# Optimization experiments

Hardware: AMD Instinct MI355X
Metric: run time of the kernel (lower is better)

The kernel has to match this reference:

```python
import jax, jax.numpy as jnp
import numpy as np

D = 128
BITS = 3
N_LEVELS = 1 << BITS  # 8
BATCH = 262144
EPS = 1e-8


def _rotation_matrix(skew_params):
    """Cayley map: A skew-symmetric from strict-upper-tri params, R = (I+A)^{-1}(I-A)."""
    iu = np.triu_indices(D, k=1)
    A = jnp.zeros((D, D), dtype=skew_params.dtype).at[iu].set(skew_params)
    A = A - A.T
    I = jnp.eye(D, dtype=skew_params.dtype)
    # torch.linalg.solve(I + A, I - A) -> R with (I + A) @ R = (I - A)
    return jnp.linalg.solve(I + A, I - A)


def setup_inputs() -> dict:
    key = jax.random.key(0)
    k1, k2, k3 = jax.random.split(key, 3)
    x = jax.random.normal(k1, (BATCH, D), dtype=jnp.float32)
    # small init so Cayley rotation stays well-conditioned (torch init is zeros)
    skew_params = jax.random.normal(k2, (D * (D - 1) // 2,), dtype=jnp.float32) * 0.05
    # Lloyd-Max centroids are a sorted 1-D codebook of 2^bits levels
    centroids = jnp.sort(jax.random.normal(k3, (N_LEVELS,), dtype=jnp.float32))
    running_mean = jnp.zeros((D,), dtype=jnp.float32)
    return {"x": x, "skew_params": skew_params, "centroids": centroids,
            "running_mean": running_mean}


def reference(x, skew_params, centroids, running_mean):
    R = _rotation_matrix(skew_params)                      # (D, D) orthogonal
    mean = jax.lax.stop_gradient(running_mean)             # buffer, detached in torch
    x_c = x - mean                                         # (B, D)
    norms = jnp.maximum(jnp.linalg.norm(x_c, axis=-1, keepdims=True), EPS)
    x_unit = x_c / norms
    x_rot = x_unit @ R.T                                   # rotate
    # STE quantize: argmin-distance gather == one_hot @ centroids
    idx = jnp.argmin(jnp.abs(x_rot[..., None] - centroids), axis=-1)  # (B, D)
    x_quant = x_rot - jax.lax.stop_gradient(x_rot) + jnp.take(centroids, idx)
    x_recon = (x_quant @ R) * norms + mean                 # unrotate, rescale, recenter
    return x_recon
```

## Files before the change

### kernel.cpp

```cpp
#include <hip/hip_runtime.h>

#define BATCH 262144
#define MARGIN 1e-5f
#define LIST_CAP (1u<<20)

typedef __attribute__((ext_vector_type(8))) short short8;
typedef __attribute__((ext_vector_type(16))) float f32x16;


__device__ __forceinline__ unsigned f2bf(float f) {
  unsigned u = __float_as_uint(f);
  return (u + 0x7FFFu + ((u >> 16) & 1u)) >> 16;
}

__global__ __attribute__((amdgpu_waves_per_eu(4, 4))) __launch_bounds__(1024)
void kpre(const float* __restrict__ skew, const float* __restrict__ x,
          const float* __restrict__ mean, double* __restrict__ M64,
          double* __restrict__ Y64, float* __restrict__ normg,
          float* __restrict__ invg, unsigned int* __restrict__ counter)
{
  const int tid = threadIdx.x;

  if (blockIdx.x != 0) {
    const int b  = blockIdx.x - 1;
    const int wv = tid >> 6, ln = tid & 63;
    const int rowbase = b*1024 + wv*64;
    const float2 mv = *(const float2*)(mean + 2*ln);
    for (int i = 0; i < 64; ++i) {
      const int row = rowbase + i;
      float2 xv = *(const float2*)(x + (size_t)row*128 + 2*ln);
      float a = xv.x - mv.x, c = xv.y - mv.y;
      float sq = fmaf(a, a, c*c);
      sq += __shfl_xor(sq, 1);  sq += __shfl_xor(sq, 2);  sq += __shfl_xor(sq, 4);
      sq += __shfl_xor(sq, 8);  sq += __shfl_xor(sq, 16); sq += __shfl_xor(sq, 32);
      if (ln == 0) {
        float n = fmaxf(sqrtf(sq), 1e-8f);
        normg[row] = n;
        invg[row]  = 1.0f / n;
      }
    }
    return;
  }

  __shared__ float colk[2][128];
  __shared__ float pivrow[128];
  const int i = tid >> 3;
  const int s = tid & 7;
  if (tid == 0) *counter = 0;

  float M[16];
  #pragma unroll
  for (int e = 0; e < 16; ++e) {
    int j = s + 8*e;
    float v;
    if (i == j)      v = 1.0f;
    else if (i < j)  v =  skew[i*127 - (i*(i-1))/2 + (j - i - 1)];
    else             v = -skew[j*127 - (j*(j-1))/2 + (i - j - 1)];
    M[e] = v;
    M64[i*128 + j] = (double)v;
  }
  if (s == 0) colk[0][i] = M[0];
  __syncthreads();

  for (int k = 0; k < 128; ++k) {
    const int p = k & 1, np = p ^ 1;
    const int ns = (k + 1) & 7, ne = (k + 1) >> 3;
    if (i == k) {
      float rec = 1.0f / colk[p][k];
      #pragma unroll
      for (int e = 0; e < 16; ++e) {
        int j = s + 8*e;
        float v = (j == k) ? 1.0f : M[e];
        v *= rec;
        M[e] = v;
        pivrow[j] = v;
      }
      if (s == ns && k < 127) colk[np][i] = M[ne];
    }
    __syncthreads();
    if (i != k) {
      float f = colk[p][i];
      #pragma unroll
      for (int e = 0; e < 16; ++e) {
        int j = s + 8*e;
        float v = (j == k) ? 0.0f : M[e];
        M[e] = fmaf(-f, pivrow[j], v);
      }
      if (s == ns && k < 127) colk[np][i] = M[ne];
    }
    __syncthreads();
  }

  #pragma unroll
  for (int e = 0; e < 16; ++e) {
    int j = s + 8*e;
    Y64[i*128 + j] = (double)M[e];
  }
}

__global__ __launch_bounds__(256, 2)
void kref(const double* __restrict__ M64, const double* __restrict__ Yin,
          double* __restrict__ Yout, double* __restrict__ Rt64,
          unsigned short* __restrict__ img, const int final_pass)
{
  __shared__ double Yc[128][17];
  __shared__ double T[128][17];
  const int t = threadIdx.x;
  const int c0 = blockIdx.x * 16;

  #pragma unroll
  for (int u = 0; u < 8; ++u) {
    int idx = u*256 + t;
    int row = idx >> 4, cc = idx & 15;
    Yc[row][cc] = Yin[row*128 + c0 + cc];
  }
  __syncthreads();

  const int m = t >> 1;
  const int h = (t & 1) * 8;

  double a0=0,a1=0,a2=0,a3=0,a4=0,a5=0,a6=0,a7=0;
  for (int j = 0; j < 128; ++j) {
    double mv = M64[m*128 + j];
    a0 = fma(mv, Yc[j][h+0], a0);  a1 = fma(mv, Yc[j][h+1], a1);
    a2 = fma(mv, Yc[j][h+2], a2);  a3 = fma(mv, Yc[j][h+3], a3);
    a4 = fma(mv, Yc[j][h+4], a4);  a5 = fma(mv, Yc[j][h+5], a5);
    a6 = fma(mv, Yc[j][h+6], a6);  a7 = fma(mv, Yc[j][h+7], a7);
  }
  T[m][h+0]=a0; T[m][h+1]=a1; T[m][h+2]=a2; T[m][h+3]=a3;
  T[m][h+4]=a4; T[m][h+5]=a5; T[m][h+6]=a6; T[m][h+7]=a7;
  __syncthreads();

  double b0=0,b1=0,b2=0,b3=0,b4=0,b5=0,b6=0,b7=0;
  for (int j = 0; j < 128; ++j) {
    double yv = Yin[m*128 + j];
    b0 = fma(yv, T[j][h+0], b0);  b1 = fma(yv, T[j][h+1], b1);
    b2 = fma(yv, T[j][h+2], b2);  b3 = fma(yv, T[j][h+3], b3);
    b4 = fma(yv, T[j][h+4], b4);  b5 = fma(yv, T[j][h+5], b5);
    b6 = fma(yv, T[j][h+6], b6);  b7 = fma(yv, T[j][h+7], b7);
  }

  double y2[8] = { 2.0*Yc[m][h+0]-b0, 2.0*Yc[m][h+1]-b1, 2.0*Yc[m][h+2]-b2,
                   2.0*Yc[m][h+3]-b3, 2.0*Yc[m][h+4]-b4, 2.0*Yc[m][h+5]-b5,
                   2.0*Yc[m][h+6]-b6, 2.0*Yc[m][h+7]-b7 };

  if (!final_pass) {
    #pragma unroll
    for (int c = 0; c < 8; ++c) Yout[m*128 + c0 + h + c] = y2[c];
  } else {
    #pragma unroll
    for (int c = 0; c < 8; ++c) {
      const int i = m, j = c0 + h + c;
      double v = 2.0*y2[c] - ((i == j) ? 1.0 : 0.0);
      Rt64[j*128 + i] = v;
      float r32 = (float)v;
      unsigned hh = f2bf(r32);
      unsigned ll = f2bf(r32 - __uint_as_float(hh << 16));
      int off1 = (((i>>5)*8 + (j>>4))*64 + ((((j>>3)&1)<<5) | (i&31)))*8 + (j&7);
      img[off1]          = (unsigned short)hh;
      img[16384 + off1]  = (unsigned short)ll;
      int off2 = (((j>>5)*8 + (i>>4))*64 + ((((i>>3)&1)<<5) | (j&31)))*8 + (i&7);
      img[32768 + off2]  = (unsigned short)hh;
      img[49152 + off2]  = (unsigned short)ll;
    }
  }
}

#define MM3(ACC, XH, XL, BH, BL)                                        \
  ACC = __builtin_amdgcn_mfma_f32_32x32x16_bf16(XH, BH, ACC, 0, 0, 0);  \
  ACC = __builtin_amdgcn_mfma_f32_32x32x16_bf16(XL, BH, ACC, 0, 0, 0);  \
  ACC = __builtin_amdgcn_mfma_f32_32x32x16_bf16(XH, BL, ACC, 0, 0, 0);

#define LGKM_BAR()                                                      \
  asm volatile("s_waitcnt lgkmcnt(0)" ::: "memory");                    \
  __builtin_amdgcn_s_barrier();                                         \
  __builtin_amdgcn_sched_barrier(0);

__global__ __launch_bounds__(256, 2)
void kmain(const float* __restrict__ x, const float* __restrict__ mean,
           const float* __restrict__ cent, const unsigned short* __restrict__ img,
           const float* __restrict__ normg, const float* __restrict__ invg,
           float* __restrict__ out,
           unsigned int* __restrict__ counter, unsigned int* __restrict__ list)
{
  __shared__ __align__(16) unsigned short Xh[2][32*128];
  __shared__ __align__(16) unsigned short Xl[2][32*128];
  __shared__ __align__(16) unsigned short Qh[2][32*128];
  __shared__ __align__(16) unsigned short Ql[2][32*128];
  __shared__ float norms[4][32];
  __shared__ float invs[4][32];

  const int tid = threadIdx.x, lane = tid & 63, w = tid >> 6;
  const int al = lane & 31, ah = lane >> 5;

  short8 B1h[8], B1l[8], B2h[8], B2l[8];
  #pragma unroll
  for (int t = 0; t < 8; ++t) {
    size_t o = (size_t)((w*8 + t)*64 + lane)*8;
    B1h[t] = *(const short8*)(img +         o);
    B1l[t] = *(const short8*)(img + 16384 + o);
    B2h[t] = *(const short8*)(img + 32768 + o);
    B2l[t] = *(const short8*)(img + 49152 + o);
  }

  const float c0 = cent[0], c1 = cent[1], c2 = cent[2], c3 = cent[3];
  const float c4 = cent[4], c5 = cent[5], c6 = cent[6], c7 = cent[7];
  const float mid0 = 0.5f*(c0+c1), mid1 = 0.5f*(c1+c2), mid2 = 0.5f*(c2+c3),
              mid3 = 0.5f*(c3+c4), mid4 = 0.5f*(c4+c5), mid5 = 0.5f*(c5+c6),
              mid6 = 0.5f*(c6+c7);
  unsigned qt0, qt1, qt2, qt3, qt4, qt5, qt6, qt7;
  {
    #define PS(C, QT) { unsigned h = f2bf(C); float hf = __uint_as_float(h<<16); \
                        QT = (h<<16) | f2bf((C) - hf); }
    PS(c0,qt0) PS(c1,qt1) PS(c2,qt2) PS(c3,qt3)
    PS(c4,qt4) PS(c5,qt5) PS(c6,qt6) PS(c7,qt7)
    #undef PS
  }

  const float2 mean2 = *(const float2*)(mean + 2*lane);
  const float meanv = mean[w*32 + al];

  const int row0 = blockIdx.x * 256;

  float2 xpf[8];
  #pragma unroll
  for (int rr = 0; rr < 8; ++rr)
    xpf[rr] = *(const float2*)(x + (size_t)(row0 + w*8 + rr)*128 + 2*lane);

  for (int ch = 0; ch < 8; ++ch) {
    const int chb = row0 + ch*32;
    const int p = ch & 1;

    if (ah == 0) {
      norms[w][al] = normg[chb + al];
      invs[w][al]  = invg[chb + al];
    }
    float2 xn[8];
    if (ch < 7) {
      #pragma unroll
      for (int rr = 0; rr < 8; ++rr)
        xn[rr] = *(const float2*)(x + (size_t)(chb + 32 + w*8 + rr)*128 + 2*lane);
    }
    #pragma unroll
    for (int rr = 0; rr < 8; ++rr) {
      const int r = w*8 + rr;
      float a = xpf[rr].x - mean2.x;
      float b = xpf[rr].y - mean2.y;
      unsigned ph, pl;
      asm("v_cvt_pk_bf16_f32 %0, %1, %2" : "=v"(ph) : "v"(a), "v"(b));
      float ha = __uint_as_float(ph << 16);
      float hb = __uint_as_float(ph & 0xFFFF0000u);
      float ra = a - ha, rb = b - hb;
      asm("v_cvt_pk_bf16_f32 %0, %1, %2" : "=v"(pl) : "v"(ra), "v"(rb));
      unsigned off = ((unsigned)(r*256 + 4*lane)) ^ (((unsigned)(r & 7)) << 4);
      *(unsigned*)((char*)&Xh[p][0] + off) = ph;
      *(unsigned*)((char*)&Xl[p][0] + off) = pl;
    }
    #pragma unroll
    for (int rr = 0; rr < 8; ++rr) xpf[rr] = xn[rr];
    LGKM_BAR();

    f32x16 accA, accB;
    #pragma unroll
    for (int g = 0; g < 16; ++g) { accA[g] = 0.0f; accB[g] = 0.0f; }
    __builtin_amdgcn_s_setprio(1);
    #pragma unroll
    for (int t = 0; t < 8; ++t) {
      unsigned fb = ((unsigned)(al*256 + t*32 + ah*16)) ^ (((unsigned)(al & 7)) << 4);
      short8 xh = *(const short8*)((const char*)&Xh[p][0] + fb);
      short8 xl = *(const short8*)((const char*)&Xl[p][0] + fb);
      if (t & 1) { MM3(accB, xh, xl, B1h[t], B1l[t]); }
      else       { MM3(accA, xh, xl, B1h[t], B1l[t]); }
    }
    __builtin_amdgcn_s_setprio(0);
    #pragma unroll
    for (int g = 0; g < 16; ++g) accA[g] += accB[g];

    unsigned qp[16];
    unsigned flags = 0;
    #pragma unroll
    for (int g = 0; g < 16; ++g) {
      const int r = (g & 3) + 8*(g >> 2) + 4*ah;
      float xr = accA[g] * invs[w][r];
      unsigned q = qt0;
      q = (xr > mid0) ? qt1 : q;  q = (xr > mid1) ? qt2 : q;
      q = (xr > mid2) ? qt3 : q;  q = (xr > mid3) ? qt4 : q;
      q = (xr > mid4) ? qt5 : q;  q = (xr > mid5) ? qt6 : q;
      q = (xr > mid6) ? qt7 : q;
      float dm = fabsf(xr - mid0);
      dm = fminf(dm, fabsf(xr - mid1)); dm = fminf(dm, fabsf(xr - mid2));
      dm = fminf(dm, fabsf(xr - mid3)); dm = fminf(dm, fabsf(xr - mid4));
      dm = fminf(dm, fabsf(xr - mid5)); dm = fminf(dm, fabsf(xr - mid6));
      qp[g] = q;
      flags |= (dm < MARGIN) ? (1u << g) : 0u;
    }
    #pragma unroll
    for (int g = 0; g < 16; ++g) {
      const int rq = (g & 3) + 8*(g >> 2) + 4*ah;
      unsigned off = ((unsigned)(rq*256 + (w*32 + al)*2)) ^ (((unsigned)(rq & 7)) << 4);
      *(unsigned short*)((char*)&Qh[p][0] + off) = (unsigned short)(qp[g] >> 16);
      *(unsigned short*)((char*)&Ql[p][0] + off) = (unsigned short)(qp[g] & 0xFFFFu);
    }
    if (__builtin_amdgcn_ballot_w64(flags != 0)) {
      #pragma unroll
      for (int g = 0; g < 16; ++g) {
        unsigned long long b = __ballot((flags >> g) & 1u);
        if (b) {
          const int rq = (g & 3) + 8*(g >> 2) + 4*ah;
          unsigned base = 0;
          if (lane == 0) base = atomicAdd(counter, (unsigned)__popcll(b));
          base = (unsigned)__shfl((int)base, 0);
          if ((flags >> g) & 1u) {
            unsigned pp = base + (unsigned)__popcll(b & ((1ull << lane) - 1ull));
            if (pp < LIST_CAP) list[pp] = (unsigned)(chb + rq);
          }
        }
      }
    }
    LGKM_BAR();

    f32x16 acc2, acc3;
    #pragma unroll
    for (int g = 0; g < 16; ++g) { acc2[g] = 0.0f; acc3[g] = 0.0f; }
    __builtin_amdgcn_s_setprio(1);
    #pragma unroll
    for (int t = 0; t < 8; ++t) {
      unsigned fb = ((unsigned)(al*256 + t*32 + ah*16)) ^ (((unsigned)(al & 7)) << 4);
      short8 xh = *(const short8*)((const char*)&Qh[p][0] + fb);
      short8 xl = *(const short8*)((const char*)&Ql[p][0] + fb);
      if (t & 1) { MM3(acc3, xh, xl, B2h[t], B2l[t]); }
      else       { MM3(acc2, xh, xl, B2h[t], B2l[t]); }
    }
    __builtin_amdgcn_s_setprio(0);

    #pragma unroll
    for (int g = 0; g < 16; ++g) {
      const int rq = (g & 3) + 8*(g >> 2) + 4*ah;
      float o = fmaf(acc2[g] + acc3[g], norms[w][rq], meanv);
      out[(size_t)(chb + rq)*128 + w*32 + al] = o;
    }
  }
}

__global__ __launch_bounds__(256)
void kfix(const float* __restrict__ x, const float* __restrict__ mean,
          const float* __restrict__ cent, const double* __restrict__ Rt64,
          float* __restrict__ out,
          const unsigned int* __restrict__ counter,
          const unsigned int* __restrict__ list)
{
  __shared__ double xs[4][128];
  __shared__ double qs[4][128];
  const int tid = threadIdx.x, lane = tid & 63, w = tid >> 6;

  unsigned cnt = *counter;
  if (cnt > LIST_CAP) cnt = LIST_CAP;

  const double cc0 = (double)cent[0], cc1 = (double)cent[1], cc2 = (double)cent[2],
               cc3 = (double)cent[3], cc4 = (double)cent[4], cc5 = (double)cent[5],
               cc6 = (double)cent[6], cc7 = (double)cent[7];
  const double m0 = 0.5*(cc0+cc1), m1 = 0.5*(cc1+cc2), m2 = 0.5*(cc2+cc3),
               m3 = 0.5*(cc3+cc4), m4 = 0.5*(cc4+cc5), m5 = 0.5*(cc5+cc6),
               m6 = 0.5*(cc6+cc7);

  const unsigned gw = blockIdx.x*4 + w, stride = gridDim.x*4;
  for (unsigned e = gw; e < cnt; e += stride) {
    const int row = (int)list[e];
    const float* xr = x + (size_t)row*128;
    const int j0 = 2*lane;

    double a = (double)xr[j0]   - (double)mean[j0];
    double b = (double)xr[j0+1] - (double)mean[j0+1];
    double s = a*a + b*b;
    s += __shfl_xor(s, 1);  s += __shfl_xor(s, 2);  s += __shfl_xor(s, 4);
    s += __shfl_xor(s, 8);  s += __shfl_xor(s, 16); s += __shfl_xor(s, 32);
    double n = sqrt(s);
    if (n < 1e-8) n = 1e-8;
    double inv = 1.0 / n;
    xs[w][j0]   = a * inv;
    xs[w][j0+1] = b * inv;
    asm volatile("s_waitcnt lgkmcnt(0)" ::: "memory");

    double acc0 = 0.0, acc1 = 0.0;
    for (int j = 0; j < 128; ++j) {
      double xj = xs[w][j];
      acc0 = fma(xj, Rt64[j*128 + j0],     acc0);
      acc1 = fma(xj, Rt64[j*128 + j0 + 1], acc1);
    }
    double q0 = cc0;
    q0 = (acc0 > m0) ? cc1 : q0;  q0 = (acc0 > m1) ? cc2 : q0;
    q0 = (acc0 > m2) ? cc3 : q0;  q0 = (acc0 > m3) ? cc4 : q0;
    q0 = (acc0 > m4) ? cc5 : q0;  q0 = (acc0 > m5) ? cc6 : q0;
    q0 = (acc0 > m6) ? cc7 : q0;
    double q1 = cc0;
    q1 = (acc1 > m0) ? cc1 : q1;  q1 = (acc1 > m1) ? cc2 : q1;
    q1 = (acc1 > m2) ? cc3 : q1;  q1 = (acc1 > m3) ? cc4 : q1;
    q1 = (acc1 > m4) ? cc5 : q1;  q1 = (acc1 > m5) ? cc6 : q1;
    q1 = (acc1 > m6) ? cc7 : q1;
    qs[w][j0]   = q0;
    qs[w][j0+1] = q1;
    asm volatile("s_waitcnt lgkmcnt(0)" ::: "memory");

    double o0 = 0.0, o1 = 0.0;
    for (int k = 0; k < 128; ++k) {
      double qk = qs[w][k];
      o0 = fma(qk, Rt64[j0*128 + k],       o0);
      o1 = fma(qk, Rt64[(j0+1)*128 + k],   o1);
    }
    out[(size_t)row*128 + j0]   = (float)fma(o0, n, (double)mean[j0]);
    out[(size_t)row*128 + j0+1] = (float)fma(o1, n, (double)mean[j0+1]);
  }
}

extern "C" void kernel_launch(void* const* d_in, const int* in_sizes, int n_in,
                              void* d_out, int out_size, void* d_ws, size_t ws_size,
                              hipStream_t stream)
{
  (void)in_sizes; (void)n_in; (void)out_size; (void)ws_size;
  const float* x    = (const float*)d_in[0];
  const float* skew = (const float*)d_in[1];
  const float* cent = (const float*)d_in[2];
  const float* mean = (const float*)d_in[3];
  float* out = (float*)d_out;

  char* ws = (char*)d_ws;
  double*         Rt64  = (double*)(ws);
  unsigned short* img   = (unsigned short*)(ws + 131072);
  unsigned int*   cntr  = (unsigned int*)(ws + 262144);
  unsigned int*   list  = (unsigned int*)(ws + 262912);
  double*         M64   = (double*)(ws + 4457216);
  double*         Y64   = (double*)(ws + 4588288);
  double*         Yb    = (double*)(ws + 4719360);
  float*          normg = (float*)(ws + 4850432);
  float*          invg  = (float*)(ws + 5899008);

  kpre <<<dim3(257),  dim3(1024), 0, stream>>>(skew, x, mean, M64, Y64,
                                               normg, invg, cntr);
  kref <<<dim3(8),    dim3(256),  0, stream>>>(M64, Y64, Yb, Rt64, img, 0);
  kref <<<dim3(8),    dim3(256),  0, stream>>>(M64, Yb, Y64, Rt64, img, 1);
  kmain<<<dim3(1024), dim3(256),  0, stream>>>(x, mean, cent, img, normg, invg,
                                               out, cntr, list);
  kfix <<<dim3(256),  dim3(256),  0, stream>>>(x, mean, cent, Rt64, out, cntr, list);
}
```

Baseline: 248.4 us.

## Reload second-GEMM weights per chunk and single-buffer LDS to fit three blocks

The second-stage rotation fragments (B2h/B2l) are no longer held in registers for the whole kernel. They are reloaded from global memory inside each chunk's second MFMA loop, and an asm barrier on the pointer keeps the compiler from hoisting those loads back out. The LDS X/Q staging buffers drop from double to single buffering, and launch bounds ask for three blocks per CU instead of two. The aim is higher occupancy to hide latency, at the cost of repeated weight loads from L2 on every chunk.

```diff
diff --git a/kernel.cpp b/kernel.cpp
--- a/kernel.cpp
+++ b/kernel.cpp
@@ -176,31 +176,29 @@
   __builtin_amdgcn_s_barrier();                                         \
   __builtin_amdgcn_sched_barrier(0);
 
-__global__ __launch_bounds__(256, 2)
+__global__ __launch_bounds__(256, 3)
 void kmain(const float* __restrict__ x, const float* __restrict__ mean,
            const float* __restrict__ cent, const unsigned short* __restrict__ img,
            const float* __restrict__ normg, const float* __restrict__ invg,
            float* __restrict__ out,
            unsigned int* __restrict__ counter, unsigned int* __restrict__ list)
 {
-  __shared__ __align__(16) unsigned short Xh[2][32*128];
-  __shared__ __align__(16) unsigned short Xl[2][32*128];
-  __shared__ __align__(16) unsigned short Qh[2][32*128];
-  __shared__ __align__(16) unsigned short Ql[2][32*128];
+  __shared__ __align__(16) unsigned short Xh[32*128];
+  __shared__ __align__(16) unsigned short Xl[32*128];
+  __shared__ __align__(16) unsigned short Qh[32*128];
+  __shared__ __align__(16) unsigned short Ql[32*128];
   __shared__ float norms[4][32];
   __shared__ float invs[4][32];
 
   const int tid = threadIdx.x, lane = tid & 63, w = tid >> 6;
   const int al = lane & 31, ah = lane >> 5;
 
-  short8 B1h[8], B1l[8], B2h[8], B2l[8];
+  short8 B1h[8], B1l[8];
   #pragma unroll
   for (int t = 0; t < 8; ++t) {
     size_t o = (size_t)((w*8 + t)*64 + lane)*8;
     B1h[t] = *(const short8*)(img +         o);
     B1l[t] = *(const short8*)(img + 16384 + o);
-    B2h[t] = *(const short8*)(img + 32768 + o);
-    B2l[t] = *(const short8*)(img + 49152 + o);
   }
 
   const float c0 = cent[0], c1 = cent[1], c2 = cent[2], c3 = cent[3];
@@ -229,7 +227,6 @@
 
   for (int ch = 0; ch < 8; ++ch) {
     const int chb = row0 + ch*32;
-    const int p = ch & 1;
 
     if (ah == 0) {
       norms[w][al] = normg[chb + al];
@@ -253,8 +250,8 @@
       float ra = a - ha, rb = b - hb;
       asm("v_cvt_pk_bf16_f32 %0, %1, %2" : "=v"(pl) : "v"(ra), "v"(rb));
       unsigned off = ((unsigned)(r*256 + 4*lane)) ^ (((unsigned)(r & 7)) << 4);
-      *(unsigned*)((char*)&Xh[p][0] + off) = ph;
-      *(unsigned*)((char*)&Xl[p][0] + off) = pl;
+      *(unsigned*)((char*)Xh + off) = ph;
+      *(unsigned*)((char*)Xl + off) = pl;
     }
     #pragma unroll
     for (int rr = 0; rr < 8; ++rr) xpf[rr] = xn[rr];
@@ -267,8 +264,8 @@
     #pragma unroll
     for (int t = 0; t < 8; ++t) {
       unsigned fb = ((unsigned)(al*256 + t*32 + ah*16)) ^ (((unsigned)(al & 7)) << 4);
-      short8 xh = *(const short8*)((const char*)&Xh[p][0] + fb);
-      short8 xl = *(const short8*)((const char*)&Xl[p][0] + fb);
+      short8 xh = *(const short8*)((const char*)Xh + fb);
+      short8 xl = *(const short8*)((const char*)Xl + fb);
       if (t & 1) { MM3(accB, xh, xl, B1h[t], B1l[t]); }
       else       { MM3(accA, xh, xl, B1h[t], B1l[t]); }
     }
@@ -298,8 +295,8 @@
     for (int g = 0; g < 16; ++g) {
       const int rq = (g & 3) + 8*(g >> 2) + 4*ah;
       unsigned off = ((unsigned)(rq*256 + (w*32 + al)*2)) ^ (((unsigned)(rq & 7)) << 4);
-      *(unsigned short*)((char*)&Qh[p][0] + off) = (unsigned short)(qp[g] >> 16);
-      *(unsigned short*)((char*)&Ql[p][0] + off) = (unsigned short)(qp[g] & 0xFFFFu);
+      *(unsigned short*)((char*)Qh + off) = (unsigned short)(qp[g] >> 16);
+      *(unsigned short*)((char*)Ql + off) = (unsigned short)(qp[g] & 0xFFFFu);
     }
     if (__builtin_amdgcn_ballot_w64(flags != 0)) {
       #pragma unroll
@@ -319,17 +316,22 @@
     }
     LGKM_BAR();
 
+    const unsigned short* i2p = img;
+    asm volatile("" : "+v"(i2p));
     f32x16 acc2, acc3;
     #pragma unroll
     for (int g = 0; g < 16; ++g) { acc2[g] = 0.0f; acc3[g] = 0.0f; }
     __builtin_amdgcn_s_setprio(1);
     #pragma unroll
     for (int t = 0; t < 8; ++t) {
+      size_t o = (size_t)((w*8 + t)*64 + lane)*8;
+      short8 bh = *(const short8*)(i2p + 32768 + o);
+      short8 bl = *(const short8*)(i2p + 49152 + o);
       unsigned fb = ((unsigned)(al*256 + t*32 + ah*16)) ^ (((unsigned)(al & 7)) << 4);
-      short8 xh = *(const short8*)((const char*)&Qh[p][0] + fb);
-      short8 xl = *(const short8*)((const char*)&Ql[p][0] + fb);
-      if (t & 1) { MM3(acc3, xh, xl, B2h[t], B2l[t]); }
-      else       { MM3(acc2, xh, xl, B2h[t], B2l[t]); }
+      short8 xh = *(const short8*)((const char*)Qh + fb);
+      short8 xl = *(const short8*)((const char*)Ql + fb);
+      if (t & 1) { MM3(acc3, xh, xl, bh, bl); }
+      else       { MM3(acc2, xh, xl, bh, bl); }
     }
     __builtin_amdgcn_s_setprio(0);
 
```

Measured after the change: 345.4 us. 1.39x slower.

## Halve barriers in Gauss-Jordan inverse by broadcasting unscaled next pivot row

Applied to the files above, without the earlier changes.

The in-block Gauss-Jordan elimination used to compute the Cayley rotation now needs one barrier per pivot step instead of two. Each non-pivot row reads the raw pivot row, which the next pivot row writes during the previous step into a double-buffered shared array, and scales it by the reciprocal on the fly. The column mapping also changes from strided to contiguous 16-element chunks per thread, so pivot-row data can be moved with float4 shared loads and stores. The trade-off is slightly different rounding, an extra multiply per row, and more shared-memory bookkeeping. This serial block is only a small part of the total kernel time.

```diff
diff --git a/kernel.cpp b/kernel.cpp
--- a/kernel.cpp
+++ b/kernel.cpp
@@ -43,7 +43,7 @@
   }
 
   __shared__ float colk[2][128];
-  __shared__ float pivrow[128];
+  __shared__ float praw[2][8][20];
   const int i = tid >> 3;
   const int s = tid & 7;
   if (tid == 0) *counter = 0;
@@ -51,7 +51,7 @@
   float M[16];
   #pragma unroll
   for (int e = 0; e < 16; ++e) {
-    int j = s + 8*e;
+    int j = s*16 + e;
     float v;
     if (i == j)      v = 1.0f;
     else if (i < j)  v =  skew[i*127 - (i*(i-1))/2 + (j - i - 1)];
@@ -60,40 +60,52 @@
     M64[i*128 + j] = (double)v;
   }
   if (s == 0) colk[0][i] = M[0];
+  if (i == 0) {
+    *(float4*)&praw[0][s][0]  = make_float4(M[0],  M[1],  M[2],  M[3]);
+    *(float4*)&praw[0][s][4]  = make_float4(M[4],  M[5],  M[6],  M[7]);
+    *(float4*)&praw[0][s][8]  = make_float4(M[8],  M[9],  M[10], M[11]);
+    *(float4*)&praw[0][s][12] = make_float4(M[12], M[13], M[14], M[15]);
+  }
   __syncthreads();
 
   for (int k = 0; k < 128; ++k) {
     const int p = k & 1, np = p ^ 1;
-    const int ns = (k + 1) & 7, ne = (k + 1) >> 3;
+    const int kp1 = k + 1;
+    const int ns = kp1 >> 4, ne = kp1 & 15;
+    const float rec = 1.0f / colk[p][k];
     if (i == k) {
-      float rec = 1.0f / colk[p][k];
       #pragma unroll
       for (int e = 0; e < 16; ++e) {
-        int j = s + 8*e;
-        float v = (j == k) ? 1.0f : M[e];
-        v *= rec;
-        M[e] = v;
-        pivrow[j] = v;
+        int j = s*16 + e;
+        M[e] = (j == k) ? rec : M[e] * rec;
       }
-      if (s == ns && k < 127) colk[np][i] = M[ne];
-    }
-    __syncthreads();
-    if (i != k) {
-      float f = colk[p][i];
+    } else {
+      const float t = colk[p][i] * rec;
+      float4 p0 = *(float4*)&praw[p][s][0];
+      float4 p1 = *(float4*)&praw[p][s][4];
+      float4 p2 = *(float4*)&praw[p][s][8];
+      float4 p3 = *(float4*)&praw[p][s][12];
+      float pr[16] = { p0.x,p0.y,p0.z,p0.w, p1.x,p1.y,p1.z,p1.w,
+                       p2.x,p2.y,p2.z,p2.w, p3.x,p3.y,p3.z,p3.w };
       #pragma unroll
       for (int e = 0; e < 16; ++e) {
-        int j = s + 8*e;
-        float v = (j == k) ? 0.0f : M[e];
-        M[e] = fmaf(-f, pivrow[j], v);
+        int j = s*16 + e;
+        M[e] = (j == k) ? (0.0f - t) : fmaf(-t, pr[e], M[e]);
       }
-      if (s == ns && k < 127) colk[np][i] = M[ne];
-    }
+      if (i == kp1) {
+        *(float4*)&praw[np][s][0]  = make_float4(M[0],  M[1],  M[2],  M[3]);
+        *(float4*)&praw[np][s][4]  = make_float4(M[4],  M[5],  M[6],  M[7]);
+        *(float4*)&praw[np][s][8]  = make_float4(M[8],  M[9],  M[10], M[11]);
+        *(float4*)&praw[np][s][12] = make_float4(M[12], M[13], M[14], M[15]);
+      }
+    }
+    if (s == ns) colk[np][i] = M[ne];
     __syncthreads();
   }
 
   #pragma unroll
   for (int e = 0; e < 16; ++e) {
-    int j = s + 8*e;
+    int j = s*16 + e;
     Y64[i*128 + j] = (double)M[e];
   }
 }
```

New measurement: 275.3 us. 10.8% more time.
